# Optimization experiments

Measured on AMD Instinct MI355X. Metric: run time of the kernel, lower is better.

The kernel has to match this reference:

```python
import jax, jax.numpy as jnp
import numpy as np

N_E = 8192
E_DIM = 256
N_TOK = 32768
MU = 0.25  # commitment weight; beta=0 so diversity loss is skipped


def setup_inputs() -> dict:
    key = jax.random.key(0)
    k1, k2, k3 = jax.random.split(key, 3)
    x = jax.random.normal(k1, (N_TOK, E_DIM), dtype=jnp.float32)
    # codebook init: uniform(-1/n_e, 1/n_e) as in the torch module
    emb = jax.random.uniform(k2, (N_E, E_DIM), dtype=jnp.float32,
                             minval=-1.0 / N_E, maxval=1.0 / N_E)
    label = jax.random.randint(k3, (N_TOK,), 0, 10, dtype=jnp.int32)
    return {"x": x, "emb": emb, "label": label, "idx": 0}


def reference(x, emb, label, idx):
    # latent: [N, e_dim]
    latent = x.reshape(-1, emb.shape[1])
    # pairwise squared distances via norm + matmul: [N, n_e]
    d = (jnp.sum(latent * latent, axis=1, keepdims=True)
         + jnp.sum(emb * emb, axis=1)[None, :]
         - 2.0 * (latent @ emb.T))
    indices = jnp.argmin(d, axis=-1)                 # [N]
    x_q = emb[indices].reshape(x.shape)              # gather
    commitment_loss = jnp.mean(jnp.square(jax.lax.stop_gradient(x_q) - x))
    codebook_loss = jnp.mean(jnp.square(x_q - jax.lax.stop_gradient(x)))
    loss = codebook_loss + MU * commitment_loss      # beta=0 -> no diversity term
    x_q_out = x + jax.lax.stop_gradient(x_q - x)     # straight-through estimator
    return x_q_out, loss, indices.reshape(x.shape[:-1])
```

## Files before the change

kernel.cpp:

```cpp
#include <hip/hip_runtime.h>
#include <float.h>
#include <stdint.h>

#define N_TOK 32768
#define N_E   8192
#define EDIM  256
#define MU_W  0.25f
#define NSPLIT 4
#define NRANGE 2048
#define BMr 128
#define MARGIN_F 4096.0f
#define OFFSETF (-0x1p21f)
#define XSCALE 512.0f
#define ESCALE -131072.0f

typedef _Float16 f16;
typedef _Float16 f16x8 __attribute__((ext_vector_type(8)));
typedef _Float16 f16x4 __attribute__((ext_vector_type(4)));
typedef float f32x4 __attribute__((ext_vector_type(4)));
typedef unsigned int u32;
typedef unsigned long long u64;

#define WS_EMB16   0
#define WS_SX      4194304
#define WS_SE      4325376
#define WS_SE25    4358144
#define WS_CAND    4390912
#define WS_PART    6488064
#define WS_RCNT    6619136
#define WS_RLIST   6619392
#define WS_RBEST   6750464

__device__ inline void gload_lds16(const void* g, void* l) {
  __builtin_amdgcn_global_load_lds(
      (const __attribute__((address_space(1))) unsigned int*)g,
      (__attribute__((address_space(3))) unsigned int*)l, 16, 0, 0);
}

__device__ inline u32 umax_(u32 a, u32 b) { return a > b ? a : b; }
__device__ inline u32 umin_(u32 a, u32 b) { return a < b ? a : b; }

__device__ inline u32 med3u(u32 a, u32 b, u32 c) {
  u32 r;
  asm("v_med3_u32 %0, %1, %2, %3" : "=v"(r) : "v"(a), "v"(b), "v"(c));
  return r;
}

__device__ inline void ins4max(u32 v, u32& a, u32& b, u32& c, u32& d) {
  u32 na = umax_(a, v);
  u32 nb = med3u(a, b, v);
  u32 nc = med3u(b, c, v);
  u32 nd = med3u(c, d, v);
  a = na; b = nb; c = nc; d = nd;
}

__global__ void zero_kernel(u32* p) { p[0] = 0u; }

__global__ __launch_bounds__(256) void conv_kernel(const float* __restrict__ src,
                                                   char* __restrict__ dst16,
                                                   float* __restrict__ norms,
                                                   float* __restrict__ norms25,
                                                   float scale, int write16, int nrows) {
  int wave = threadIdx.x >> 6;
  int lane = threadIdx.x & 63;
  int row = blockIdx.x * 4 + wave;
  if (row >= nrows) return;
  const float4 v = *(const float4*)(src + (size_t)row * EDIM + lane * 4);
  float s = (v.x * v.x + v.y * v.y) + (v.z * v.z + v.w * v.w);
#pragma unroll
  for (int off = 32; off >= 1; off >>= 1) s += __shfl_xor(s, off);
  if (lane == 0) {
    norms[row] = s;
    if (norms25) norms25[row] = s * 0x1p25f;
  }
  if (write16) {
    f16x4 h;
    h[0] = (f16)(v.x * scale); h[1] = (f16)(v.y * scale);
    h[2] = (f16)(v.z * scale); h[3] = (f16)(v.w * scale);
    *(f16x4*)(dst16 + (size_t)(row >> 4) * 8192 + (lane >> 1) * 256 +
              (row & 15) * 16 + (lane & 1) * 8) = h;
  }
}

__global__ __launch_bounds__(512, 2) void vq_main(const float* __restrict__ x,
                                                  const char* __restrict__ e16,
                                                  const float* __restrict__ se25,
                                                  u32* __restrict__ cand) {
  __shared__ __align__(16) char Abuf[128 * 512];
  __shared__ __align__(16) char Bbuf[2 * 32768];
  __shared__ u32 scratch[8][4][16][4];

  const int tid = threadIdx.x;
  const int lane = tid & 63;
  const int wid = tid >> 6;
  const int wm = wid >> 2;
  const int wn = wid & 3;
  const int l15 = lane & 15;
  const int lg  = lane >> 4;
  const int split = blockIdx.x & 3;
  const int bm = (blockIdx.x >> 2) * BMr;
  const int nbase = split * NRANGE;

  int aOff[4], bOff[4];
#pragma unroll
  for (int mi = 0; mi < 4; ++mi) aOff[mi] = (wm * 4 + mi) * 8192 + lg * 256 + l15 * 16;
#pragma unroll
  for (int ni = 0; ni < 4; ++ni) bOff[ni] = (wn * 4 + ni) * 2048 + lg * 256 + l15 * 16;

  int svo[4], sdo[4];
#pragma unroll
  for (int j = 0; j < 4; ++j) {
    int i = j * 512 + tid;
    svo[j] = (i >> 7) * 8192 + (i & 127) * 16;
    sdo[j] = i * 16;
  }

  {
    const int row = tid >> 2, seg = tid & 3;
    const float4* xs = (const float4*)(x + (size_t)(bm + row) * EDIM + seg * 64);
    const int abase = (row >> 4) * 8192 + (row & 15) * 16;
#pragma unroll
    for (int u = 0; u < 8; ++u) {
      float4 a0 = xs[2 * u], a1 = xs[2 * u + 1];
      f16x8 hv;
      hv[0] = (f16)(a0.x * XSCALE); hv[1] = (f16)(a0.y * XSCALE);
      hv[2] = (f16)(a0.z * XSCALE); hv[3] = (f16)(a0.w * XSCALE);
      hv[4] = (f16)(a1.x * XSCALE); hv[5] = (f16)(a1.y * XSCALE);
      hv[6] = (f16)(a1.z * XSCALE); hv[7] = (f16)(a1.w * XSCALE);
      *(f16x8*)&Abuf[abase + (seg * 8 + u) * 256] = hv;
    }
  }
  {
    const size_t eb = ((size_t)(nbase >> 4)) * 8192;
#pragma unroll
    for (int j = 0; j < 4; ++j) gload_lds16(e16 + eb + svo[j], &Bbuf[sdo[j]]);
  }
  __syncthreads();

  u32 d1[16], d2[16], d3[16], d4[16];
#pragma unroll
  for (int s = 0; s < 16; ++s) { d1[s] = 0u; d2[s] = 0u; d3[s] = 0u; d4[s] = 0u; }

  const int idl = wn * 64 + l15;

  for (int t = 0; t < 8; ++t) {
    float sev[4];
#pragma unroll
    for (int ni = 0; ni < 4; ++ni)
      sev[ni] = se25[nbase + t * 256 + wn * 64 + ni * 16 + l15] + OFFSETF;

    f32x4 acc[4][4];
#pragma unroll
    for (int mi = 0; mi < 4; ++mi)
#pragma unroll
      for (int ni = 0; ni < 4; ++ni)
        acc[mi][ni] = (f32x4){sev[ni], sev[ni], sev[ni], sev[ni]};

#pragma unroll
    for (int q = 0; q < 4; ++q) {
      {
        const int sn = (t * 4 + q + 1) & 31;
        const int t2 = sn >> 2, q2 = sn & 3;
        const size_t eb = ((size_t)(nbase >> 4) + t2 * 16) * 8192 + q2 * 2048;
        const int db = ((q + 1) & 1) * 32768;
#pragma unroll
        for (int j = 0; j < 4; ++j) gload_lds16(e16 + eb + svo[j], &Bbuf[db + sdo[j]]);
      }
      const int rb = (q & 1) * 32768;
#pragma unroll
      for (int kk = 0; kk < 2; ++kk) {
        f16x8 av[4], bv[4];
#pragma unroll
        for (int mi = 0; mi < 4; ++mi)
          av[mi] = *(const f16x8*)&Abuf[aOff[mi] + q * 2048 + kk * 1024];
#pragma unroll
        for (int ni = 0; ni < 4; ++ni)
          bv[ni] = *(const f16x8*)&Bbuf[rb + bOff[ni] + kk * 1024];
#pragma unroll
        for (int mi = 0; mi < 4; ++mi)
#pragma unroll
          for (int ni = 0; ni < 4; ++ni)
            acc[mi][ni] = __builtin_amdgcn_mfma_f32_16x16x32_f16(av[mi], bv[ni], acc[mi][ni], 0, 0, 0);
      }
      if (q == 3) {
#pragma unroll
        for (int ni = 0; ni < 4; ++ni) {
          const u32 id = (u32)(t * 256 + ni * 16 + idl);
#pragma unroll
          for (int mi = 0; mi < 4; ++mi)
#pragma unroll
            for (int r = 0; r < 4; ++r) {
              u32 up = (__float_as_uint(acc[mi][ni][r]) & 0xFFFFF800u) | id;
              int s = mi * 4 + r;
              ins4max(up, d1[s], d2[s], d3[s], d4[s]);
            }
        }
      }
      __syncthreads();
    }
  }

#pragma unroll
  for (int off = 8; off >= 1; off >>= 1) {
#pragma unroll
    for (int s = 0; s < 16; ++s) {
      u32 e1 = (u32)__shfl_xor((int)d1[s], off);
      u32 e2 = (u32)__shfl_xor((int)d2[s], off);
      u32 e3 = (u32)__shfl_xor((int)d3[s], off);
      u32 e4 = (u32)__shfl_xor((int)d4[s], off);
      ins4max(e1, d1[s], d2[s], d3[s], d4[s]);
      ins4max(e2, d1[s], d2[s], d3[s], d4[s]);
      ins4max(e3, d1[s], d2[s], d3[s], d4[s]);
      ins4max(e4, d1[s], d2[s], d3[s], d4[s]);
    }
  }
  if (l15 == 0) {
#pragma unroll
    for (int s = 0; s < 16; ++s) {
      scratch[wid][lg][s][0] = d1[s];
      scratch[wid][lg][s][1] = d2[s];
      scratch[wid][lg][s][2] = d3[s];
      scratch[wid][lg][s][3] = d4[s];
    }
  }
  __syncthreads();
  if (tid < 128) {
    const int row = tid;
    const int wmr = row >> 6, mi = (row >> 4) & 3, lgr = (row >> 2) & 3, rr = row & 3;
    const int s = mi * 4 + rr;
    u32 a1 = scratch[wmr * 4][lgr][s][0];
    u32 a2 = scratch[wmr * 4][lgr][s][1];
    u32 a3 = scratch[wmr * 4][lgr][s][2];
    u32 a4 = scratch[wmr * 4][lgr][s][3];
#pragma unroll
    for (int w = 1; w < 4; ++w) {
#pragma unroll
      for (int c = 0; c < 4; ++c)
        ins4max(scratch[wmr * 4 + w][lgr][s][c], a1, a2, a3, a4);
    }
    size_t base = (size_t)split * (N_TOK * 4) + (size_t)(bm + row) * 4;
    cand[base + 0] = a1; cand[base + 1] = a2; cand[base + 2] = a3; cand[base + 3] = a4;
  }
}

__global__ __launch_bounds__(256) void vq_gather_kernel(
    const float* __restrict__ x, const float* __restrict__ emb,
    const float* __restrict__ sx, const float* __restrict__ se,
    const u32* __restrict__ cand,
    float* __restrict__ out_q, float* __restrict__ out_idx,
    float* __restrict__ partials,
    u32* __restrict__ rcnt, u32* __restrict__ rlist, u64* __restrict__ rbest) {
  const int token = blockIdx.x;
  const int tid = threadIdx.x;
  __shared__ int s_j;
  __shared__ int s_cnt;
  __shared__ int s_cj[16];
  __shared__ float s_dv[16];
  __shared__ float red[4];

  if (tid == 0) {
    u32 u[16];
    float uf[16];
    float gmin = FLT_MAX;
#pragma unroll
    for (int sp = 0; sp < 4; ++sp)
#pragma unroll
      for (int c = 0; c < 4; ++c) {
        u32 v = cand[(size_t)sp * (N_TOK * 4) + (size_t)token * 4 + c];
        u[sp * 4 + c] = v;
        float f = __uint_as_float(v);
        uf[sp * 4 + c] = f;
        gmin = fminf(gmin, f);
      }
    bool guard = false;
#pragma unroll
    for (int sp = 0; sp < 4; ++sp) guard = guard || (uf[sp * 4 + 3] <= gmin + MARGIN_F);
    int cnt;
    if (guard) {
      u32 slot = atomicAdd(rcnt, 1u);
      rlist[slot] = (u32)token;
      rbest[slot] = ~0ull;
      cnt = -1;
    } else {
      cnt = 0;
#pragma unroll
      for (int sp = 0; sp < 4; ++sp)
#pragma unroll
        for (int c = 0; c < 4; ++c) {
          int k = sp * 4 + c;
          if (uf[k] <= gmin + MARGIN_F)
            s_cj[cnt++] = sp * NRANGE + (int)(u[k] & 0x7FFu);
        }
      if (cnt == 1) s_j = s_cj[0];
    }
    s_cnt = cnt;
  }
  __syncthreads();
  int cnt = s_cnt;
  if (cnt < 0) return;
  if (cnt > 1 && tid < cnt) {
    int j = s_cj[tid];
    const float* xr = x + (size_t)token * EDIM;
    const float* er = emb + (size_t)j * EDIM;
    float a = 0.f;
    for (int k = 0; k < EDIM; ++k) a = fmaf(xr[k], er[k], a);
    s_dv[tid] = (sx[token] + se[j]) - 2.0f * a;
  }
  __syncthreads();
  if (cnt > 1 && tid == 0) {
    float bd = s_dv[0]; int bj = s_cj[0];
    for (int c = 1; c < cnt; ++c) {
      float d = s_dv[c]; int j = s_cj[c];
      if (d < bd || (d == bd && j < bj)) { bd = d; bj = j; }
    }
    s_j = bj;
  }
  __syncthreads();
  const int j = s_j;
  if (tid == 0) out_idx[token] = (float)j;
  float xv = x[(size_t)token * EDIM + tid];
  float q  = emb[(size_t)j * EDIM + tid];
  float diff = q - xv;
  out_q[(size_t)token * EDIM + tid] = xv + diff;
  float sq = diff * diff;
#pragma unroll
  for (int off = 32; off >= 1; off >>= 1) sq += __shfl_xor(sq, off);
  const int wave = tid >> 6, lane = tid & 63;
  if (lane == 0) red[wave] = sq;
  __syncthreads();
  if (tid == 0) partials[token] = (red[0] + red[1]) + (red[2] + red[3]);
}

__global__ __launch_bounds__(256) void vq_rescan_scan(
    const float* __restrict__ x, const float* __restrict__ emb,
    const float* __restrict__ sx, const float* __restrict__ se,
    const u32* __restrict__ rcnt, const u32* __restrict__ rlist,
    u64* __restrict__ rbest) {
  const int tid = threadIdx.x;
  const int n = (int)rcnt[0];
  const int total = n * 32;
  __shared__ float xs[EDIM];
  __shared__ u64 rw[4];

  for (int w = blockIdx.x; w < total; w += gridDim.x) {
    const int it = w >> 5, chunk = w & 31;
    const int token = (int)rlist[it];
    __syncthreads();
    xs[tid] = x[(size_t)token * EDIM + tid];
    __syncthreads();
    const float sxt = sx[token];
    const int j = chunk * 256 + tid;
    const float* er = emb + (size_t)j * EDIM;
    float a = 0.f;
#pragma unroll 8
    for (int k4 = 0; k4 < 64; ++k4) {
      float4 e4 = ((const float4*)er)[k4];
      float4 x4 = ((const float4*)xs)[k4];
      a = fmaf(x4.x, e4.x, a);
      a = fmaf(x4.y, e4.y, a);
      a = fmaf(x4.z, e4.z, a);
      a = fmaf(x4.w, e4.w, a);
    }
    float d = (sxt + se[j]) - 2.0f * a;
    u64 pk = ((u64)__float_as_uint(d) << 32) | (u32)j;
    const int lane = tid & 63, wave = tid >> 6;
#pragma unroll
    for (int off = 32; off >= 1; off >>= 1) {
      u64 o = __shfl_xor(pk, off);
      pk = o < pk ? o : pk;
    }
    if (lane == 0) rw[wave] = pk;
    __syncthreads();
    if (tid == 0) {
      u64 b = rw[0];
#pragma unroll
      for (int ww = 1; ww < 4; ++ww) b = rw[ww] < b ? rw[ww] : b;
      atomicMin(rbest + it, b);
    }
  }
}

__global__ __launch_bounds__(256) void vq_rescan_write(
    const float* __restrict__ x, const float* __restrict__ emb,
    const u32* __restrict__ rcnt, const u32* __restrict__ rlist,
    const u64* __restrict__ rbest,
    float* __restrict__ out_q, float* __restrict__ out_idx,
    float* __restrict__ partials) {
  const int tid = threadIdx.x;
  const int n = (int)rcnt[0];
  __shared__ float red[4];

  for (int it = blockIdx.x; it < n; it += gridDim.x) {
    const int token = (int)rlist[it];
    const int j = (int)(u32)(rbest[it] & 0xFFFFFFFFull);
    if (tid == 0) out_idx[token] = (float)j;
    float xv = x[(size_t)token * EDIM + tid];
    float q  = emb[(size_t)j * EDIM + tid];
    float diff = q - xv;
    out_q[(size_t)token * EDIM + tid] = xv + diff;
    float sq = diff * diff;
#pragma unroll
    for (int off = 32; off >= 1; off >>= 1) sq += __shfl_xor(sq, off);
    const int lane = tid & 63, wave = tid >> 6;
    __syncthreads();
    if (lane == 0) red[wave] = sq;
    __syncthreads();
    if (tid == 0) partials[token] = (red[0] + red[1]) + (red[2] + red[3]);
  }
}

__global__ __launch_bounds__(256) void vq_loss_kernel(const float* __restrict__ partials,
                                                      float* __restrict__ loss_out) {
  const int tid = threadIdx.x;
  float s = 0.f;
  for (int i = tid; i < N_TOK; i += 256) s += partials[i];
  __shared__ float red[4];
#pragma unroll
  for (int off = 32; off >= 1; off >>= 1) s += __shfl_xor(s, off);
  const int wave = tid >> 6, lane = tid & 63;
  if (lane == 0) red[wave] = s;
  __syncthreads();
  if (tid == 0) {
    float tot = (red[0] + red[1]) + (red[2] + red[3]);
    float mean = tot / (float)(N_TOK * EDIM);
    loss_out[0] = mean + MU_W * mean;
  }
}

extern "C" void kernel_launch(void* const* d_in, const int* in_sizes, int n_in,
                              void* d_out, int out_size, void* d_ws, size_t ws_size,
                              hipStream_t stream) {
  const float* x   = (const float*)d_in[0];
  const float* emb = (const float*)d_in[1];

  float* out      = (float*)d_out;
  float* out_q    = out;
  float* out_loss = out + (size_t)N_TOK * EDIM;
  float* out_idx  = out_loss + 1;

  char* w = (char*)d_ws;
  char*  emb16    = w + WS_EMB16;
  float* sx       = (float*)(w + WS_SX);
  float* se       = (float*)(w + WS_SE);
  float* se25     = (float*)(w + WS_SE25);
  u32*   cand     = (u32*)(w + WS_CAND);
  float* partials = (float*)(w + WS_PART);
  u32*   rcnt     = (u32*)(w + WS_RCNT);
  u32*   rlist    = (u32*)(w + WS_RLIST);
  u64*   rbest    = (u64*)(w + WS_RBEST);

  zero_kernel<<<1, 1, 0, stream>>>(rcnt);
  conv_kernel<<<N_E / 4, 256, 0, stream>>>(emb, emb16, se, se25, ESCALE, 1, N_E);
  conv_kernel<<<N_TOK / 4, 256, 0, stream>>>(x, nullptr, sx, nullptr, XSCALE, 0, N_TOK);

  vq_main<<<NSPLIT * (N_TOK / BMr), 512, 0, stream>>>(x, emb16, se25, cand);

  vq_gather_kernel<<<N_TOK, 256, 0, stream>>>(x, emb, sx, se, cand, out_q, out_idx, partials,
                                              rcnt, rlist, rbest);
  vq_rescan_scan<<<2048, 256, 0, stream>>>(x, emb, sx, se, rcnt, rlist, rbest);
  vq_rescan_write<<<64, 256, 0, stream>>>(x, emb, rcnt, rlist, rbest, out_q, out_idx, partials);
  vq_loss_kernel<<<1, 256, 0, stream>>>(partials, out_loss);
}
```

Baseline: 341.9 us.

## Split codebook prefetch into half-chunks with vmcnt waits and finer barriers

Restructures the main GEMM loop's codebook streaming. Each K-chunk is now loaded as two half-chunks, with explicit s_waitcnt vmcnt(4) plus raw s_barrier instead of a full __syncthreads after each chunk, so global-to-LDS loads stay in flight across the MFMA work. It also raises wave priority around the MFMA bursts and moves the per-code norm load off the accumulator-init path, adding it only at candidate selection. The tighter manual synchronisation risks LDS hazards if the counts are wrong, and the extra barriers could add stalls.

```diff
diff --git a/kernel.cpp b/kernel.cpp
--- a/kernel.cpp
+++ b/kernel.cpp
@@ -100,6 +100,7 @@
   const int split = blockIdx.x & 3;
   const int bm = (blockIdx.x >> 2) * BMr;
   const int nbase = split * NRANGE;
+  const int splitRB = split * 128;
 
   int aOff[4], bOff[4];
 #pragma unroll
@@ -107,12 +108,12 @@
 #pragma unroll
   for (int ni = 0; ni < 4; ++ni) bOff[ni] = (wn * 4 + ni) * 2048 + lg * 256 + l15 * 16;
 
-  int svo[4], sdo[4];
-#pragma unroll
-  for (int j = 0; j < 4; ++j) {
-    int i = j * 512 + tid;
-    svo[j] = (i >> 7) * 8192 + (i & 127) * 16;
-    sdo[j] = i * 16;
+  int svo2[2], sdo2[2];
+#pragma unroll
+  for (int l = 0; l < 2; ++l) {
+    int u = l * 512 + tid;
+    svo2[l] = (u >> 6) * 8192 + (u & 63) * 16;
+    sdo2[l] = (u >> 6) * 2048 + (u & 63) * 16;
   }
 
   {
@@ -130,12 +131,14 @@
       *(f16x8*)&Abuf[abase + (seg * 8 + u) * 256] = hv;
     }
   }
-  {
-    const size_t eb = ((size_t)(nbase >> 4)) * 8192;
-#pragma unroll
-    for (int j = 0; j < 4; ++j) gload_lds16(e16 + eb + svo[j], &Bbuf[sdo[j]]);
-  }
-  __syncthreads();
+  __syncthreads();
+
+#pragma unroll
+  for (int h = 0; h < 2; ++h) {
+    const size_t eb = (size_t)splitRB * 8192 + h * 1024;
+#pragma unroll
+    for (int l = 0; l < 2; ++l) gload_lds16(e16 + eb + svo2[l], &Bbuf[h * 1024 + sdo2[l]]);
+  }
 
   u32 d1[16], d2[16], d3[16], d4[16];
 #pragma unroll
@@ -145,43 +148,67 @@
 
   for (int t = 0; t < 8; ++t) {
     float sev[4];
-#pragma unroll
-    for (int ni = 0; ni < 4; ++ni)
-      sev[ni] = se25[nbase + t * 256 + wn * 64 + ni * 16 + l15] + OFFSETF;
-
     f32x4 acc[4][4];
 #pragma unroll
     for (int mi = 0; mi < 4; ++mi)
 #pragma unroll
       for (int ni = 0; ni < 4; ++ni)
-        acc[mi][ni] = (f32x4){sev[ni], sev[ni], sev[ni], sev[ni]};
+        acc[mi][ni] = (f32x4){OFFSETF, OFFSETF, OFFSETF, OFFSETF};
 
 #pragma unroll
     for (int q = 0; q < 4; ++q) {
+      const int c = t * 4 + q;
+      const int cn = (c + 1) & 31;
+      const int t2 = cn >> 2, q2 = cn & 3;
+      const size_t ebN = (size_t)(splitRB + t2 * 16) * 8192 + q2 * 2048;
+      const int dbN = (cn & 1) * 32768;
+      const int rb = (q & 1) * 32768;
+
+#pragma unroll
+      for (int l = 0; l < 2; ++l) gload_lds16(e16 + ebN + svo2[l], &Bbuf[dbN + sdo2[l]]);
+      if (q == 2) {
+#pragma unroll
+        for (int ni = 0; ni < 4; ++ni)
+          sev[ni] = se25[nbase + t * 256 + wn * 64 + ni * 16 + l15];
+      }
+      asm volatile("s_waitcnt vmcnt(4)" ::: "memory");
+      __builtin_amdgcn_s_barrier();
+      __builtin_amdgcn_sched_barrier(0);
       {
-        const int sn = (t * 4 + q + 1) & 31;
-        const int t2 = sn >> 2, q2 = sn & 3;
-        const size_t eb = ((size_t)(nbase >> 4) + t2 * 16) * 8192 + q2 * 2048;
-        const int db = ((q + 1) & 1) * 32768;
-#pragma unroll
-        for (int j = 0; j < 4; ++j) gload_lds16(e16 + eb + svo[j], &Bbuf[db + sdo[j]]);
-      }
-      const int rb = (q & 1) * 32768;
-#pragma unroll
-      for (int kk = 0; kk < 2; ++kk) {
         f16x8 av[4], bv[4];
 #pragma unroll
-        for (int mi = 0; mi < 4; ++mi)
-          av[mi] = *(const f16x8*)&Abuf[aOff[mi] + q * 2048 + kk * 1024];
-#pragma unroll
-        for (int ni = 0; ni < 4; ++ni)
-          bv[ni] = *(const f16x8*)&Bbuf[rb + bOff[ni] + kk * 1024];
+        for (int mi = 0; mi < 4; ++mi) av[mi] = *(const f16x8*)&Abuf[aOff[mi] + q * 2048];
+#pragma unroll
+        for (int ni = 0; ni < 4; ++ni) bv[ni] = *(const f16x8*)&Bbuf[rb + bOff[ni]];
+        __builtin_amdgcn_s_setprio(1);
 #pragma unroll
         for (int mi = 0; mi < 4; ++mi)
 #pragma unroll
           for (int ni = 0; ni < 4; ++ni)
             acc[mi][ni] = __builtin_amdgcn_mfma_f32_16x16x32_f16(av[mi], bv[ni], acc[mi][ni], 0, 0, 0);
+        __builtin_amdgcn_s_setprio(0);
       }
+
+#pragma unroll
+      for (int l = 0; l < 2; ++l) gload_lds16(e16 + ebN + 1024 + svo2[l], &Bbuf[dbN + 1024 + sdo2[l]]);
+      asm volatile("s_waitcnt vmcnt(4)" ::: "memory");
+      __builtin_amdgcn_s_barrier();
+      __builtin_amdgcn_sched_barrier(0);
+      {
+        f16x8 av[4], bv[4];
+#pragma unroll
+        for (int mi = 0; mi < 4; ++mi) av[mi] = *(const f16x8*)&Abuf[aOff[mi] + q * 2048 + 1024];
+#pragma unroll
+        for (int ni = 0; ni < 4; ++ni) bv[ni] = *(const f16x8*)&Bbuf[rb + bOff[ni] + 1024];
+        __builtin_amdgcn_s_setprio(1);
+#pragma unroll
+        for (int mi = 0; mi < 4; ++mi)
+#pragma unroll
+          for (int ni = 0; ni < 4; ++ni)
+            acc[mi][ni] = __builtin_amdgcn_mfma_f32_16x16x32_f16(av[mi], bv[ni], acc[mi][ni], 0, 0, 0);
+        __builtin_amdgcn_s_setprio(0);
+      }
+
       if (q == 3) {
 #pragma unroll
         for (int ni = 0; ni < 4; ++ni) {
@@ -190,15 +217,16 @@
           for (int mi = 0; mi < 4; ++mi)
 #pragma unroll
             for (int r = 0; r < 4; ++r) {
-              u32 up = (__float_as_uint(acc[mi][ni][r]) & 0xFFFFF800u) | id;
+              u32 up = (__float_as_uint(acc[mi][ni][r] + sev[ni]) & 0xFFFFF800u) | id;
               int s = mi * 4 + r;
               ins4max(up, d1[s], d2[s], d3[s], d4[s]);
             }
         }
       }
-      __syncthreads();
-    }
-  }
+    }
+  }
+
+  __syncthreads();
 
 #pragma unroll
   for (int off = 8; off >= 1; off >>= 1) {
```

Result: faster. 327.0 us (-4.4%).

## Restructure VQ distance kernel into 64-row tiles with triple-buffered B pipeline

Applied to the files above, without the earlier changes.

The main distance kernel moves from 128-row tiles with 512 threads to 64-row tiles with 256 threads (four waves split along N). The codebook stream now uses a three-slot buffer with one barrier per 16-wide K chunk, controlled by an explicit vmcnt wait, and the MFMA section runs at raised priority. The codebook-norm bias is added after accumulation rather than used as the initial accumulator value. Separately, the zero kernel and the two conversion kernels are merged into a single launch to cut launch overhead. The smaller tile halves A reuse per block and doubles the number of blocks, so codebook reloads from L2 increase.

```diff
diff --git a/kernel.cpp b/kernel.cpp
--- a/kernel.cpp
+++ b/kernel.cpp
@@ -8,7 +8,7 @@
 #define MU_W  0.25f
 #define NSPLIT 4
 #define NRANGE 2048
-#define BMr 128
+#define BMr 64
 #define MARGIN_F 4096.0f
 #define OFFSETF (-0x1p21f)
 #define XSCALE 512.0f
@@ -54,71 +54,74 @@
   a = na; b = nb; c = nc; d = nd;
 }
 
-__global__ void zero_kernel(u32* p) { p[0] = 0u; }
-
-__global__ __launch_bounds__(256) void conv_kernel(const float* __restrict__ src,
-                                                   char* __restrict__ dst16,
-                                                   float* __restrict__ norms,
-                                                   float* __restrict__ norms25,
-                                                   float scale, int write16, int nrows) {
+__global__ __launch_bounds__(256) void conv_fused(const float* __restrict__ emb,
+                                                  const float* __restrict__ x,
+                                                  char* __restrict__ dst16,
+                                                  float* __restrict__ se,
+                                                  float* __restrict__ se25,
+                                                  float* __restrict__ sx,
+                                                  u32* __restrict__ rcnt) {
+  if (blockIdx.x == 0 && threadIdx.x == 0) rcnt[0] = 0u;
   int wave = threadIdx.x >> 6;
   int lane = threadIdx.x & 63;
   int row = blockIdx.x * 4 + wave;
-  if (row >= nrows) return;
-  const float4 v = *(const float4*)(src + (size_t)row * EDIM + lane * 4);
-  float s = (v.x * v.x + v.y * v.y) + (v.z * v.z + v.w * v.w);
-#pragma unroll
-  for (int off = 32; off >= 1; off >>= 1) s += __shfl_xor(s, off);
-  if (lane == 0) {
-    norms[row] = s;
-    if (norms25) norms25[row] = s * 0x1p25f;
-  }
-  if (write16) {
+  if (row < N_E) {
+    const float4 v = *(const float4*)(emb + (size_t)row * EDIM + lane * 4);
+    float s = (v.x * v.x + v.y * v.y) + (v.z * v.z + v.w * v.w);
+#pragma unroll
+    for (int off = 32; off >= 1; off >>= 1) s += __shfl_xor(s, off);
+    if (lane == 0) { se[row] = s; se25[row] = s * 0x1p25f; }
     f16x4 h;
-    h[0] = (f16)(v.x * scale); h[1] = (f16)(v.y * scale);
-    h[2] = (f16)(v.z * scale); h[3] = (f16)(v.w * scale);
+    h[0] = (f16)(v.x * ESCALE); h[1] = (f16)(v.y * ESCALE);
+    h[2] = (f16)(v.z * ESCALE); h[3] = (f16)(v.w * ESCALE);
     *(f16x4*)(dst16 + (size_t)(row >> 4) * 8192 + (lane >> 1) * 256 +
               (row & 15) * 16 + (lane & 1) * 8) = h;
-  }
-}
-
-__global__ __launch_bounds__(512, 2) void vq_main(const float* __restrict__ x,
+  } else {
+    int xr = row - N_E;
+    const float4 v = *(const float4*)(x + (size_t)xr * EDIM + lane * 4);
+    float s = (v.x * v.x + v.y * v.y) + (v.z * v.z + v.w * v.w);
+#pragma unroll
+    for (int off = 32; off >= 1; off >>= 1) s += __shfl_xor(s, off);
+    if (lane == 0) sx[xr] = s;
+  }
+}
+
+__global__ __launch_bounds__(256, 2) void vq_main(const float* __restrict__ x,
                                                   const char* __restrict__ e16,
                                                   const float* __restrict__ se25,
                                                   u32* __restrict__ cand) {
-  __shared__ __align__(16) char Abuf[128 * 512];
-  __shared__ __align__(16) char Bbuf[2 * 32768];
-  __shared__ u32 scratch[8][4][16][4];
+  __shared__ __align__(16) char lds[81920];
+  char* Abuf = lds;
+  char* Bbuf = lds + 32768;
 
   const int tid = threadIdx.x;
   const int lane = tid & 63;
-  const int wid = tid >> 6;
-  const int wm = wid >> 2;
-  const int wn = wid & 3;
+  const int wn = tid >> 6;
   const int l15 = lane & 15;
   const int lg  = lane >> 4;
   const int split = blockIdx.x & 3;
   const int bm = (blockIdx.x >> 2) * BMr;
   const int nbase = split * NRANGE;
+  const int splitRB = split * 128;
 
   int aOff[4], bOff[4];
 #pragma unroll
-  for (int mi = 0; mi < 4; ++mi) aOff[mi] = (wm * 4 + mi) * 8192 + lg * 256 + l15 * 16;
-#pragma unroll
-  for (int ni = 0; ni < 4; ++ni) bOff[ni] = (wn * 4 + ni) * 2048 + lg * 256 + l15 * 16;
+  for (int mi = 0; mi < 4; ++mi) aOff[mi] = mi * 8192 + lg * 256 + l15 * 16;
+#pragma unroll
+  for (int ni = 0; ni < 4; ++ni) bOff[ni] = (wn * 4 + ni) * 1024 + lg * 256 + l15 * 16;
 
   int svo[4], sdo[4];
 #pragma unroll
-  for (int j = 0; j < 4; ++j) {
-    int i = j * 512 + tid;
-    svo[j] = (i >> 7) * 8192 + (i & 127) * 16;
-    sdo[j] = i * 16;
+  for (int l = 0; l < 4; ++l) {
+    int u = l * 256 + tid;
+    svo[l] = (u >> 6) * 8192 + (u & 63) * 16;
+    sdo[l] = (u >> 6) * 1024 + (u & 63) * 16;
   }
 
   {
     const int row = tid >> 2, seg = tid & 3;
     const float4* xs = (const float4*)(x + (size_t)(bm + row) * EDIM + seg * 64);
-    const int abase = (row >> 4) * 8192 + (row & 15) * 16;
+    const int ab = (row >> 4) * 8192 + (row & 15) * 16;
 #pragma unroll
     for (int u = 0; u < 8; ++u) {
       float4 a0 = xs[2 * u], a1 = xs[2 * u + 1];
@@ -127,13 +130,13 @@
       hv[2] = (f16)(a0.z * XSCALE); hv[3] = (f16)(a0.w * XSCALE);
       hv[4] = (f16)(a1.x * XSCALE); hv[5] = (f16)(a1.y * XSCALE);
       hv[6] = (f16)(a1.z * XSCALE); hv[7] = (f16)(a1.w * XSCALE);
-      *(f16x8*)&Abuf[abase + (seg * 8 + u) * 256] = hv;
+      *(f16x8*)&Abuf[ab + (seg * 8 + u) * 256] = hv;
     }
   }
   {
-    const size_t eb = ((size_t)(nbase >> 4)) * 8192;
-#pragma unroll
-    for (int j = 0; j < 4; ++j) gload_lds16(e16 + eb + svo[j], &Bbuf[sdo[j]]);
+    const size_t eb = (size_t)splitRB * 8192;
+#pragma unroll
+    for (int l = 0; l < 4; ++l) gload_lds16(e16 + eb + svo[l], Bbuf + sdo[l]);
   }
   __syncthreads();
 
@@ -143,62 +146,68 @@
 
   const int idl = wn * 64 + l15;
 
+  int bufc = 0;
   for (int t = 0; t < 8; ++t) {
     float sev[4];
 #pragma unroll
     for (int ni = 0; ni < 4; ++ni)
-      sev[ni] = se25[nbase + t * 256 + wn * 64 + ni * 16 + l15] + OFFSETF;
+      sev[ni] = se25[nbase + t * 256 + wn * 64 + ni * 16 + l15];
 
     f32x4 acc[4][4];
 #pragma unroll
     for (int mi = 0; mi < 4; ++mi)
 #pragma unroll
       for (int ni = 0; ni < 4; ++ni)
-        acc[mi][ni] = (f32x4){sev[ni], sev[ni], sev[ni], sev[ni]};
-
-#pragma unroll
-    for (int q = 0; q < 4; ++q) {
+        acc[mi][ni] = (f32x4){OFFSETF, OFFSETF, OFFSETF, OFFSETF};
+
+#pragma unroll
+    for (int q = 0; q < 8; ++q) {
+      const int c = t * 8 + q;
+      const int cn = (c + 1) & 63;
+      const int tn = cn >> 3, qn = cn & 7;
+      const int bufn = (bufc == 2) ? 0 : bufc + 1;
       {
-        const int sn = (t * 4 + q + 1) & 31;
-        const int t2 = sn >> 2, q2 = sn & 3;
-        const size_t eb = ((size_t)(nbase >> 4) + t2 * 16) * 8192 + q2 * 2048;
-        const int db = ((q + 1) & 1) * 32768;
-#pragma unroll
-        for (int j = 0; j < 4; ++j) gload_lds16(e16 + eb + svo[j], &Bbuf[db + sdo[j]]);
+        const size_t ebN = (size_t)(splitRB + tn * 16) * 8192 + qn * 1024;
+        char* dstN = Bbuf + bufn * 16384;
+#pragma unroll
+        for (int l = 0; l < 4; ++l) gload_lds16(e16 + ebN + svo[l], dstN + sdo[l]);
       }
-      const int rb = (q & 1) * 32768;
-#pragma unroll
-      for (int kk = 0; kk < 2; ++kk) {
+      asm volatile("s_waitcnt vmcnt(4)" ::: "memory");
+      __builtin_amdgcn_s_barrier();
+      __builtin_amdgcn_sched_barrier(0);
+      {
+        const char* Bc = Bbuf + bufc * 16384;
         f16x8 av[4], bv[4];
 #pragma unroll
-        for (int mi = 0; mi < 4; ++mi)
-          av[mi] = *(const f16x8*)&Abuf[aOff[mi] + q * 2048 + kk * 1024];
-#pragma unroll
-        for (int ni = 0; ni < 4; ++ni)
-          bv[ni] = *(const f16x8*)&Bbuf[rb + bOff[ni] + kk * 1024];
+        for (int mi = 0; mi < 4; ++mi) av[mi] = *(const f16x8*)&Abuf[aOff[mi] + q * 1024];
+#pragma unroll
+        for (int ni = 0; ni < 4; ++ni) bv[ni] = *(const f16x8*)&Bc[bOff[ni]];
+        __builtin_amdgcn_s_setprio(1);
 #pragma unroll
         for (int mi = 0; mi < 4; ++mi)
 #pragma unroll
           for (int ni = 0; ni < 4; ++ni)
             acc[mi][ni] = __builtin_amdgcn_mfma_f32_16x16x32_f16(av[mi], bv[ni], acc[mi][ni], 0, 0, 0);
+        __builtin_amdgcn_s_setprio(0);
       }
-      if (q == 3) {
-#pragma unroll
-        for (int ni = 0; ni < 4; ++ni) {
-          const u32 id = (u32)(t * 256 + ni * 16 + idl);
-#pragma unroll
-          for (int mi = 0; mi < 4; ++mi)
-#pragma unroll
-            for (int r = 0; r < 4; ++r) {
-              u32 up = (__float_as_uint(acc[mi][ni][r]) & 0xFFFFF800u) | id;
-              int s = mi * 4 + r;
-              ins4max(up, d1[s], d2[s], d3[s], d4[s]);
-            }
+      bufc = bufn;
+    }
+
+#pragma unroll
+    for (int ni = 0; ni < 4; ++ni) {
+      const u32 id = (u32)(t * 256 + ni * 16 + idl);
+#pragma unroll
+      for (int mi = 0; mi < 4; ++mi)
+#pragma unroll
+        for (int r = 0; r < 4; ++r) {
+          u32 up = (__float_as_uint(acc[mi][ni][r] + sev[ni]) & 0xFFFFF800u) | id;
+          int s = mi * 4 + r;
+          ins4max(up, d1[s], d2[s], d3[s], d4[s]);
         }
-      }
-      __syncthreads();
-    }
-  }
+    }
+  }
+
+  __syncthreads();
 
 #pragma unroll
   for (int off = 8; off >= 1; off >>= 1) {
@@ -214,29 +223,30 @@
       ins4max(e4, d1[s], d2[s], d3[s], d4[s]);
     }
   }
+  u32 (*scratch)[4][16][4] = (u32 (*)[4][16][4])lds;
   if (l15 == 0) {
 #pragma unroll
     for (int s = 0; s < 16; ++s) {
-      scratch[wid][lg][s][0] = d1[s];
-      scratch[wid][lg][s][1] = d2[s];
-      scratch[wid][lg][s][2] = d3[s];
-      scratch[wid][lg][s][3] = d4[s];
-    }
-  }
-  __syncthreads();
-  if (tid < 128) {
+      scratch[wn][lg][s][0] = d1[s];
+      scratch[wn][lg][s][1] = d2[s];
+      scratch[wn][lg][s][2] = d3[s];
+      scratch[wn][lg][s][3] = d4[s];
+    }
+  }
+  __syncthreads();
+  if (tid < 64) {
     const int row = tid;
-    const int wmr = row >> 6, mi = (row >> 4) & 3, lgr = (row >> 2) & 3, rr = row & 3;
+    const int mi = row >> 4, lgr = (row >> 2) & 3, rr = row & 3;
     const int s = mi * 4 + rr;
-    u32 a1 = scratch[wmr * 4][lgr][s][0];
-    u32 a2 = scratch[wmr * 4][lgr][s][1];
-    u32 a3 = scratch[wmr * 4][lgr][s][2];
-    u32 a4 = scratch[wmr * 4][lgr][s][3];
+    u32 a1 = scratch[0][lgr][s][0];
+    u32 a2 = scratch[0][lgr][s][1];
+    u32 a3 = scratch[0][lgr][s][2];
+    u32 a4 = scratch[0][lgr][s][3];
 #pragma unroll
     for (int w = 1; w < 4; ++w) {
 #pragma unroll
       for (int c = 0; c < 4; ++c)
-        ins4max(scratch[wmr * 4 + w][lgr][s][c], a1, a2, a3, a4);
+        ins4max(scratch[w][lgr][s][c], a1, a2, a3, a4);
     }
     size_t base = (size_t)split * (N_TOK * 4) + (size_t)(bm + row) * 4;
     cand[base + 0] = a1; cand[base + 1] = a2; cand[base + 2] = a3; cand[base + 3] = a4;
@@ -449,11 +459,9 @@
   u32*   rlist    = (u32*)(w + WS_RLIST);
   u64*   rbest    = (u64*)(w + WS_RBEST);
 
-  zero_kernel<<<1, 1, 0, stream>>>(rcnt);
-  conv_kernel<<<N_E / 4, 256, 0, stream>>>(emb, emb16, se, se25, ESCALE, 1, N_E);
-  conv_kernel<<<N_TOK / 4, 256, 0, stream>>>(x, nullptr, sx, nullptr, XSCALE, 0, N_TOK);
-
-  vq_main<<<NSPLIT * (N_TOK / BMr), 512, 0, stream>>>(x, emb16, se25, cand);
+  conv_fused<<<(N_E + N_TOK) / 4, 256, 0, stream>>>(emb, x, emb16, se, se25, sx, rcnt);
+
+  vq_main<<<NSPLIT * (N_TOK / BMr), 256, 0, stream>>>(x, emb16, se25, cand);
 
   vq_gather_kernel<<<N_TOK, 256, 0, stream>>>(x, emb, sx, se, cand, out_q, out_idx, partials,
                                               rcnt, rlist, rbest);
```

Result: faster. 314.8 us (-7.9%).
